# Optimization experiments

Hardware: AMD Instinct MI355X
Metric: run time of the kernel (lower is better)

The kernel has to match this reference:

```python
import jax, jax.numpy as jnp
import numpy as np

WIDTHS = list(range(5, 50, 5))    # 9 widths
SIGMAS = list(range(2, 22, 2))    # 10 sigmas -> 90 filters
KMAX = 45                          # pad all kernels to max width
SUB_LOW_RATIO = 1.0
TOPK = 64


def _build_kernels():
    # Normalized 1D Gaussian kernels, zero-padded to KMAX and centered.
    # Zero taps contribute nothing, so SAME-padded conv matches per-width conv.
    ks = []
    for w in WIDTHS:
        for s in SIGMAS:
            x = np.arange(w, dtype=np.float32) - (w - 1) / 2.0
            g = np.exp(-x * x / (2.0 * s * s)).astype(np.float32)
            g /= g.sum()
            pad = np.zeros(KMAX, np.float32)
            off = (KMAX - w) // 2
            pad[off:off + w] = g
            ks.append(pad)
    return jnp.asarray(np.stack(ks))  # [90, KMAX]


def setup_inputs() -> dict:
    key = jax.random.key(0)
    k1, k2, k3 = jax.random.split(key, 3)
    return {
        "image": jax.random.normal(k1, (4, 3, 256, 256), jnp.float32),
        "kernels": _build_kernels(),                                   # fixed Gaussian buffers
        "channel_prompt": jax.random.normal(k2, (90,), jnp.float32),   # learned gating
        "lambda_param": jax.random.normal(k3, (1,), jnp.float32) * 0.1,
    }


def _hfc_all(image, kernels):
    # image: [B,C,H,W]; kernels: [F,K]. Returns high-pass stack [F,B,C,H,W].
    B, C, H, W = image.shape
    F = kernels.shape[0]
    x = image.reshape(B * C, 1, H, W)
    kv = kernels.reshape(F, 1, KMAX, 1)   # vertical pass (per-channel -> F filters)
    kh = kernels.reshape(F, 1, 1, KMAX)   # horizontal pass (depthwise over F)
    dn = ('NCHW', 'OIHW', 'NCHW')
    y = jax.lax.conv_general_dilated(x, kv, (1, 1), 'SAME', dimension_numbers=dn)
    low = jax.lax.conv_general_dilated(y, kh, (1, 1), 'SAME',
                                       feature_group_count=F, dimension_numbers=dn)
    low = low.reshape(B, C, F, H, W).transpose(2, 0, 1, 3, 4)  # [F,B,C,H,W]
    # high-frequency component, clamped (is_clamp=True)
    return jnp.clip(image[None] - SUB_LOW_RATIO * low, -1.0, 1.0)


def reference(image, kernels, channel_prompt, lambda_param):
    lam = jax.nn.sigmoid(lambda_param)[0]
    hfc = _hfc_all(image, kernels)                 # [90,B,C,H,W]
    _, idx = jax.lax.top_k(channel_prompt, TOPK)   # select 64 experts
    top = hfc[idx]                                 # gather [64,B,C,H,W]
    # pairwise lambda mixup -> [32,B,C,H,W] (stacked list of mixed images)
    mixed = lam * top[0::2] + (1.0 - lam) * top[1::2]
    return mixed
```

## Files before the change

### kernel.cpp

```cpp
#include <hip/hip_runtime.h>
#include <hip/hip_bf16.h>
#include <math.h>

typedef __attribute__((ext_vector_type(8))) short bf16x8;
typedef __attribute__((ext_vector_type(4))) float f32x4;

#define HST 136
#define PLANE_STRIDE 92416
#define ROW_STRIDE   304

#define WS_IDX   0
#define WS_LAM   256
#define WS_FRAG  4096
#define WS_IMG   266240

#define NB_PREP 542

__device__ __forceinline__ unsigned f2bf(float f) {
    unsigned u = __builtin_bit_cast(unsigned, f);
    u += 0x7FFFu + ((u >> 16) & 1u);
    return u >> 16;
}

__device__ __forceinline__ unsigned pk2(float a, float b) {
    return f2bf(a) | (f2bf(b) << 16);
}

__global__ __launch_bounds__(128) void gmix_topk(const float* __restrict__ cp,
                                                 const float* __restrict__ lp,
                                                 int* __restrict__ idx,
                                                 float* __restrict__ lam) {
    int i = threadIdx.x;
    if (i < 90) {
        float v = cp[i];
        int rank = 0;
        for (int j = 0; j < 90; ++j) {
            float vj = cp[j];
            rank += (vj > v) || (vj == v && j < i);
        }
        if (rank < 64) idx[rank] = i;
    }
    if (i == 0) lam[0] = 1.0f / (1.0f + expf(-lp[0]));
}

__global__ __launch_bounds__(256) void gmix_prep(const float* __restrict__ img,
                                                 const float* __restrict__ kers,
                                                 const int* __restrict__ idx,
                                                 short* __restrict__ wsimg,
                                                 short* __restrict__ frag) {
    const int b   = blockIdx.x;
    const int tid = threadIdx.x;
    if (b < NB_PREP) {
        const int cid = b * 256 + tid;
        if (cid >= 12 * 304 * 38) return;
        const int plane = cid / (304 * 38);
        const int rr    = cid % (304 * 38);
        const int r     = rr / 38;
        const int ch    = rr % 38;
        uint4 o = {0u, 0u, 0u, 0u};
        const int gr = r - 22;
        if (gr >= 0 && gr < 256 && ch >= 3 && ch < 35) {
            const float* sp = img + (size_t)plane * 65536 + gr * 256 + (ch * 8 - 24);
            const float4 v0 = *(const float4*)sp;
            const float4 v1 = *(const float4*)(sp + 4);
            o.x = pk2(v0.x, v0.y);
            o.y = pk2(v0.z, v0.w);
            o.z = pk2(v1.x, v1.y);
            o.w = pk2(v1.z, v1.w);
        }
        *(uint4*)(wsimg + plane * PLANE_STRIDE + r * ROW_STRIDE + ch * 8) = o;
    } else if (tid < 64) {
        const int unit  = b - NB_PREP;
        const int fid   = unit >> 1;
        const int v     = unit & 1;
        const int f     = idx[fid];
        const int lm    = tid & 15;
        const int lg    = tid >> 4;
        const int shift = v ? 0 : 2;
        short* dst = frag + ((size_t)unit * 64 + tid) * 16;
#pragma unroll
        for (int ka = 0; ka < 2; ++ka)
#pragma unroll
            for (int e = 0; e < 8; ++e) {
                const int k = ka * 32 + lg * 8 + e;
                const int d = k - lm - shift;
                const float t = (d >= 0 && d < 45) ? kers[f * 45 + d] : 0.f;
                dst[ka * 8 + e] = (short)f2bf(t);
            }
    }
}

__global__ __launch_bounds__(512, 4) void gmix_mfma(const float* __restrict__ img,
                                                    const short* __restrict__ wsimg,
                                                    const short* __restrict__ frag,
                                                    const float* __restrict__ lamp,
                                                    float* __restrict__ out) {
    __shared__ short HT[2][128 * HST];

    const int tid  = threadIdx.x;
    const int lane = tid & 63;
    const int wv   = tid >> 6;
    const int lm   = lane & 15;
    const int lg   = lane >> 4;

    const int bid   = blockIdx.x;
    const int p     = bid / 96;
    const int rem   = bid % 96;
    const int plane = rem >> 3;
    const int band  = (rem >> 1) & 3;
    const int half  = rem & 1;
    const int r0    = band * 64;

    const float* imgp = img + (size_t)plane * 65536;
    const float  lam  = lamp[0];

    const short* fbA = frag + (size_t)(2 * p) * 2048;
    const short* fbB = fbA + 2048;
    const bf16x8 bA1_0 = *(const bf16x8*)(fbA + lane * 16);
    const bf16x8 bA1_1 = *(const bf16x8*)(fbA + lane * 16 + 8);
    const bf16x8 bA2_0 = *(const bf16x8*)(fbA + 1024 + lane * 16);
    const bf16x8 bA2_1 = *(const bf16x8*)(fbA + 1024 + lane * 16 + 8);
    const bf16x8 bB1_0 = *(const bf16x8*)(fbB + lane * 16);
    const bf16x8 bB1_1 = *(const bf16x8*)(fbB + lane * 16 + 8);
    const bf16x8 bB2_0 = *(const bf16x8*)(fbB + 1024 + lane * 16);
    const bf16x8 bB2_1 = *(const bf16x8*)(fbB + 1024 + lane * 16 + 8);

    const short* abase = wsimg + plane * PLANE_STRIDE + r0 * ROW_STRIDE + half * 128
                       + lm * ROW_STRIDE + wv * 16 + lg * 8;
    bf16x8 a0s[7], a1s[7];
#pragma unroll
    for (int t1 = 0; t1 < 7; ++t1) {
        a0s[t1] = *(const bf16x8*)(abase + t1 * 16 * ROW_STRIDE);
        a1s[t1] = *(const bf16x8*)(abase + t1 * 16 * ROW_STRIDE + 32);
    }

    short* htw = (short*)&HT[0][0] + (wv * 16 + lm) * HST + lg * 4;
#pragma unroll
    for (int t1 = 0; t1 < 7; ++t1) {
        f32x4 accA = {0.f, 0.f, 0.f, 0.f};
        f32x4 accB = {0.f, 0.f, 0.f, 0.f};
        accA = __builtin_amdgcn_mfma_f32_16x16x32_bf16(a0s[t1], bA1_0, accA, 0, 0, 0);
        accB = __builtin_amdgcn_mfma_f32_16x16x32_bf16(a0s[t1], bB1_0, accB, 0, 0, 0);
        accA = __builtin_amdgcn_mfma_f32_16x16x32_bf16(a1s[t1], bA1_1, accA, 0, 0, 0);
        accB = __builtin_amdgcn_mfma_f32_16x16x32_bf16(a1s[t1], bB1_1, accB, 0, 0, 0);
        uint2 pkA, pkB;
        pkA.x = pk2(accA[0], accA[1]);
        pkA.y = pk2(accA[2], accA[3]);
        pkB.x = pk2(accB[0], accB[1]);
        pkB.y = pk2(accB[2], accB[3]);
        *(uint2*)(htw + t1 * 16) = pkA;
        *(uint2*)(htw + 128 * HST + t1 * 16) = pkB;
    }

    const int ocol = half * 128 + wv * 16 + lg * 4;
    f32x4 ivs[4];
#pragma unroll
    for (int t = 0; t < 4; ++t)
        ivs[t] = *(const f32x4*)(imgp + (r0 + t * 16 + lm) * 256 + ocol);

    const short* htr = (const short*)&HT[0][0] + (wv * 16 + lm) * HST + lg * 8;
#pragma unroll
    for (int t = 0; t < 4; ++t) {
        const bf16x8 hA0 = *(const bf16x8*)(htr + t * 16);
        const bf16x8 hA1 = *(const bf16x8*)(htr + t * 16 + 32);
        const bf16x8 hB0 = *(const bf16x8*)(htr + 128 * HST + t * 16);
        const bf16x8 hB1 = *(const bf16x8*)(htr + 128 * HST + t * 16 + 32);
        f32x4 aA = {0.f, 0.f, 0.f, 0.f};
        f32x4 aB = {0.f, 0.f, 0.f, 0.f};
        aA = __builtin_amdgcn_mfma_f32_16x16x32_bf16(hA0, bA2_0, aA, 0, 0, 0);
        aB = __builtin_amdgcn_mfma_f32_16x16x32_bf16(hB0, bB2_0, aB, 0, 0, 0);
        aA = __builtin_amdgcn_mfma_f32_16x16x32_bf16(hA1, bA2_1, aA, 0, 0, 0);
        aB = __builtin_amdgcn_mfma_f32_16x16x32_bf16(hB1, bB2_1, aB, 0, 0, 0);

        f32x4 res;
#pragma unroll
        for (int q = 0; q < 4; ++q) {
            float hA = ivs[t][q] - aA[q];
            hA = fminf(fmaxf(hA, -1.f), 1.f);
            float hB = ivs[t][q] - aB[q];
            hB = fminf(fmaxf(hB, -1.f), 1.f);
            res[q] = lam * hA + (1.0f - lam) * hB;
        }
        float* op = out + ((size_t)(p * 12 + plane) << 16) + (r0 + t * 16 + lm) * 256 + ocol;
        *(f32x4*)op = res;
    }
}

extern "C" void kernel_launch(void* const* d_in, const int* in_sizes, int n_in,
                              void* d_out, int out_size, void* d_ws, size_t ws_size,
                              hipStream_t stream) {
    const float* image   = (const float*)d_in[0];
    const float* kernels = (const float*)d_in[1];
    const float* prompt  = (const float*)d_in[2];
    const float* lambdap = (const float*)d_in[3];
    float* out = (float*)d_out;

    int*   ws_idx  = (int*)d_ws;
    float* ws_lam  = (float*)((char*)d_ws + WS_LAM);
    short* ws_frag = (short*)((char*)d_ws + WS_FRAG);
    short* ws_img  = (short*)((char*)d_ws + WS_IMG);

    gmix_topk<<<1, 128, 0, stream>>>(prompt, lambdap, ws_idx, ws_lam);
    gmix_prep<<<NB_PREP + 128, 256, 0, stream>>>(image, kernels, ws_idx, ws_img, ws_frag);
    gmix_mfma<<<3072, 512, 0, stream>>>(image, ws_img, ws_frag, ws_lam, out);
}
```

Before: 59.20 us.

## Stage image tile in LDS and loop four filter pairs per block

Each block now copies its bf16 image window into shared memory once and reuses it across four filter pairs in a loop, and the grid shrinks from 3072 to 768 blocks. The aim is to cut repeated global/L2 reads of the same image tile and per-block setup such as the original-image loads. In exchange, blocks use more LDS, occupancy hints drop from 4 to 2, and parallelism is lower. The loop reuses the HT buffer without a barrier between iterations, which is safe only because each wave reads back just the HT rows it wrote itself.

```diff
diff --git a/kernel.cpp b/kernel.cpp
--- a/kernel.cpp
+++ b/kernel.cpp
@@ -6,8 +6,13 @@
 typedef __attribute__((ext_vector_type(4))) float f32x4;
 
 #define HST 136
+#define AST 184
 #define PLANE_STRIDE 92416
 #define ROW_STRIDE   304
+
+#define LDS_A_HALFS  20608
+#define LDS_HT_HALFS (128 * HST)
+#define LDS_BYTES    ((LDS_A_HALFS + 2 * LDS_HT_HALFS) * 2)
 
 #define WS_IDX   0
 #define WS_LAM   256
@@ -90,12 +95,14 @@
     }
 }
 
-__global__ __launch_bounds__(512, 4) void gmix_mfma(const float* __restrict__ img,
+__global__ __launch_bounds__(512, 2) void gmix_mfma(const float* __restrict__ img,
                                                     const short* __restrict__ wsimg,
                                                     const short* __restrict__ frag,
                                                     const float* __restrict__ lamp,
                                                     float* __restrict__ out) {
-    __shared__ short HT[2][128 * HST];
+    extern __shared__ short S[];
+    short* A  = S;
+    short* HT = S + LDS_A_HALFS;
 
     const int tid  = threadIdx.x;
     const int lane = tid & 63;
@@ -104,7 +111,7 @@
     const int lg   = lane >> 4;
 
     const int bid   = blockIdx.x;
-    const int p     = bid / 96;
+    const int pg    = bid / 96;
     const int rem   = bid % 96;
     const int plane = rem >> 3;
     const int band  = (rem >> 1) & 3;
@@ -114,42 +121,18 @@
     const float* imgp = img + (size_t)plane * 65536;
     const float  lam  = lamp[0];
 
-    const short* fbA = frag + (size_t)(2 * p) * 2048;
-    const short* fbB = fbA + 2048;
-    const bf16x8 bA1_0 = *(const bf16x8*)(fbA + lane * 16);
-    const bf16x8 bA1_1 = *(const bf16x8*)(fbA + lane * 16 + 8);
-    const bf16x8 bA2_0 = *(const bf16x8*)(fbA + 1024 + lane * 16);
-    const bf16x8 bA2_1 = *(const bf16x8*)(fbA + 1024 + lane * 16 + 8);
-    const bf16x8 bB1_0 = *(const bf16x8*)(fbB + lane * 16);
-    const bf16x8 bB1_1 = *(const bf16x8*)(fbB + lane * 16 + 8);
-    const bf16x8 bB2_0 = *(const bf16x8*)(fbB + 1024 + lane * 16);
-    const bf16x8 bB2_1 = *(const bf16x8*)(fbB + 1024 + lane * 16 + 8);
-
-    const short* abase = wsimg + plane * PLANE_STRIDE + r0 * ROW_STRIDE + half * 128
-                       + lm * ROW_STRIDE + wv * 16 + lg * 8;
-    bf16x8 a0s[7], a1s[7];
-#pragma unroll
-    for (int t1 = 0; t1 < 7; ++t1) {
-        a0s[t1] = *(const bf16x8*)(abase + t1 * 16 * ROW_STRIDE);
-        a1s[t1] = *(const bf16x8*)(abase + t1 * 16 * ROW_STRIDE + 32);
-    }
-
-    short* htw = (short*)&HT[0][0] + (wv * 16 + lm) * HST + lg * 4;
-#pragma unroll
-    for (int t1 = 0; t1 < 7; ++t1) {
-        f32x4 accA = {0.f, 0.f, 0.f, 0.f};
-        f32x4 accB = {0.f, 0.f, 0.f, 0.f};
-        accA = __builtin_amdgcn_mfma_f32_16x16x32_bf16(a0s[t1], bA1_0, accA, 0, 0, 0);
-        accB = __builtin_amdgcn_mfma_f32_16x16x32_bf16(a0s[t1], bB1_0, accB, 0, 0, 0);
-        accA = __builtin_amdgcn_mfma_f32_16x16x32_bf16(a1s[t1], bA1_1, accA, 0, 0, 0);
-        accB = __builtin_amdgcn_mfma_f32_16x16x32_bf16(a1s[t1], bB1_1, accB, 0, 0, 0);
-        uint2 pkA, pkB;
-        pkA.x = pk2(accA[0], accA[1]);
-        pkA.y = pk2(accA[2], accA[3]);
-        pkB.x = pk2(accB[0], accB[1]);
-        pkB.y = pk2(accB[2], accB[3]);
-        *(uint2*)(htw + t1 * 16) = pkA;
-        *(uint2*)(htw + 128 * HST + t1 * 16) = pkB;
+    {
+        const short* src = wsimg + plane * PLANE_STRIDE + r0 * ROW_STRIDE + half * 128;
+#pragma unroll
+        for (int s = 0; s < 5; ++s) {
+            const int it = s * 512 + tid;
+            if (it < 112 * 22) {
+                const int wr  = it / 22;
+                const int wc8 = it % 22;
+                const uint4 v = *(const uint4*)(src + wr * ROW_STRIDE + wc8 * 8);
+                *(uint4*)(A + wr * AST + wc8 * 8) = v;
+            }
+        }
     }
 
     const int ocol = half * 128 + wv * 16 + lg * 4;
@@ -158,31 +141,71 @@
     for (int t = 0; t < 4; ++t)
         ivs[t] = *(const f32x4*)(imgp + (r0 + t * 16 + lm) * 256 + ocol);
 
-    const short* htr = (const short*)&HT[0][0] + (wv * 16 + lm) * HST + lg * 8;
-#pragma unroll
-    for (int t = 0; t < 4; ++t) {
-        const bf16x8 hA0 = *(const bf16x8*)(htr + t * 16);
-        const bf16x8 hA1 = *(const bf16x8*)(htr + t * 16 + 32);
-        const bf16x8 hB0 = *(const bf16x8*)(htr + 128 * HST + t * 16);
-        const bf16x8 hB1 = *(const bf16x8*)(htr + 128 * HST + t * 16 + 32);
-        f32x4 aA = {0.f, 0.f, 0.f, 0.f};
-        f32x4 aB = {0.f, 0.f, 0.f, 0.f};
-        aA = __builtin_amdgcn_mfma_f32_16x16x32_bf16(hA0, bA2_0, aA, 0, 0, 0);
-        aB = __builtin_amdgcn_mfma_f32_16x16x32_bf16(hB0, bB2_0, aB, 0, 0, 0);
-        aA = __builtin_amdgcn_mfma_f32_16x16x32_bf16(hA1, bA2_1, aA, 0, 0, 0);
-        aB = __builtin_amdgcn_mfma_f32_16x16x32_bf16(hB1, bB2_1, aB, 0, 0, 0);
-
-        f32x4 res;
-#pragma unroll
-        for (int q = 0; q < 4; ++q) {
-            float hA = ivs[t][q] - aA[q];
-            hA = fminf(fmaxf(hA, -1.f), 1.f);
-            float hB = ivs[t][q] - aB[q];
-            hB = fminf(fmaxf(hB, -1.f), 1.f);
-            res[q] = lam * hA + (1.0f - lam) * hB;
-        }
-        float* op = out + ((size_t)(p * 12 + plane) << 16) + (r0 + t * 16 + lm) * 256 + ocol;
-        *(f32x4*)op = res;
+    __syncthreads();
+
+    const short* arow = A + lm * AST + wv * 16 + lg * 8;
+    short*       htw  = HT + (wv * 16 + lm) * HST + lg * 4;
+    const short* htr  = HT + (wv * 16 + lm) * HST + lg * 8;
+
+#pragma unroll 1
+    for (int i = 0; i < 4; ++i) {
+        const int p = pg * 4 + i;
+
+        const short* fbA = frag + (size_t)(2 * p) * 2048;
+        const short* fbB = fbA + 2048;
+        const bf16x8 bA1_0 = *(const bf16x8*)(fbA + lane * 16);
+        const bf16x8 bA1_1 = *(const bf16x8*)(fbA + lane * 16 + 8);
+        const bf16x8 bA2_0 = *(const bf16x8*)(fbA + 1024 + lane * 16);
+        const bf16x8 bA2_1 = *(const bf16x8*)(fbA + 1024 + lane * 16 + 8);
+        const bf16x8 bB1_0 = *(const bf16x8*)(fbB + lane * 16);
+        const bf16x8 bB1_1 = *(const bf16x8*)(fbB + lane * 16 + 8);
+        const bf16x8 bB2_0 = *(const bf16x8*)(fbB + 1024 + lane * 16);
+        const bf16x8 bB2_1 = *(const bf16x8*)(fbB + 1024 + lane * 16 + 8);
+
+#pragma unroll
+        for (int t1 = 0; t1 < 7; ++t1) {
+            const bf16x8 a0 = *(const bf16x8*)(arow + t1 * 16 * AST);
+            const bf16x8 a1 = *(const bf16x8*)(arow + t1 * 16 * AST + 32);
+            f32x4 accA = {0.f, 0.f, 0.f, 0.f};
+            f32x4 accB = {0.f, 0.f, 0.f, 0.f};
+            accA = __builtin_amdgcn_mfma_f32_16x16x32_bf16(a0, bA1_0, accA, 0, 0, 0);
+            accB = __builtin_amdgcn_mfma_f32_16x16x32_bf16(a0, bB1_0, accB, 0, 0, 0);
+            accA = __builtin_amdgcn_mfma_f32_16x16x32_bf16(a1, bA1_1, accA, 0, 0, 0);
+            accB = __builtin_amdgcn_mfma_f32_16x16x32_bf16(a1, bB1_1, accB, 0, 0, 0);
+            uint2 pkA, pkB;
+            pkA.x = pk2(accA[0], accA[1]);
+            pkA.y = pk2(accA[2], accA[3]);
+            pkB.x = pk2(accB[0], accB[1]);
+            pkB.y = pk2(accB[2], accB[3]);
+            *(uint2*)(htw + t1 * 16) = pkA;
+            *(uint2*)(htw + LDS_HT_HALFS + t1 * 16) = pkB;
+        }
+
+        float* outp = out + ((size_t)(p * 12 + plane) << 16);
+#pragma unroll
+        for (int t = 0; t < 4; ++t) {
+            const bf16x8 hA0 = *(const bf16x8*)(htr + t * 16);
+            const bf16x8 hA1 = *(const bf16x8*)(htr + t * 16 + 32);
+            const bf16x8 hB0 = *(const bf16x8*)(htr + LDS_HT_HALFS + t * 16);
+            const bf16x8 hB1 = *(const bf16x8*)(htr + LDS_HT_HALFS + t * 16 + 32);
+            f32x4 aA = {0.f, 0.f, 0.f, 0.f};
+            f32x4 aB = {0.f, 0.f, 0.f, 0.f};
+            aA = __builtin_amdgcn_mfma_f32_16x16x32_bf16(hA0, bA2_0, aA, 0, 0, 0);
+            aB = __builtin_amdgcn_mfma_f32_16x16x32_bf16(hB0, bB2_0, aB, 0, 0, 0);
+            aA = __builtin_amdgcn_mfma_f32_16x16x32_bf16(hA1, bA2_1, aA, 0, 0, 0);
+            aB = __builtin_amdgcn_mfma_f32_16x16x32_bf16(hB1, bB2_1, aB, 0, 0, 0);
+
+            f32x4 res;
+#pragma unroll
+            for (int q = 0; q < 4; ++q) {
+                float hA = ivs[t][q] - aA[q];
+                hA = fminf(fmaxf(hA, -1.f), 1.f);
+                float hB = ivs[t][q] - aB[q];
+                hB = fminf(fmaxf(hB, -1.f), 1.f);
+                res[q] = lam * hA + (1.0f - lam) * hB;
+            }
+            *(f32x4*)(outp + (r0 + t * 16 + lm) * 256 + ocol) = res;
+        }
     }
 }
 
@@ -202,5 +225,5 @@
 
     gmix_topk<<<1, 128, 0, stream>>>(prompt, lambdap, ws_idx, ws_lam);
     gmix_prep<<<NB_PREP + 128, 256, 0, stream>>>(image, kernels, ws_idx, ws_img, ws_frag);
-    gmix_mfma<<<3072, 512, 0, stream>>>(image, ws_img, ws_frag, ws_lam, out);
-}
+    gmix_mfma<<<768, 512, LDS_BYTES, stream>>>(image, ws_img, ws_frag, ws_lam, out);
+}
```

New measurement: 53.82 us. 9.1% less time.
